# Kernel optimization log

Measured on AMD Instinct MI355X. Metric: run time of the kernel, lower is better.

## Reference

```python
import jax, jax.numpy as jnp
import numpy as np

N = 50000      # nodes
E = 800000     # edges (before self-loops)
H = 4          # heads
C = 64         # hidden_unit per head
IN = 256       # input_dim
OUT = 64       # output_dim
NEG = 0.2      # LeakyReLU slope in GATConv
EPS = 1e-5     # BatchNorm eps


def setup_inputs() -> dict:
    key = jax.random.key(0)
    ks = jax.random.split(key, 12)
    s = 0.05
    HC = H * C
    return {
        'x': jax.random.normal(ks[0], (N, IN), dtype=jnp.float32),
        'edge_index': jax.random.randint(ks[1], (2, E), 0, N, dtype=jnp.int64),
        # GATConv layer 1
        'W1': jax.random.normal(ks[2], (IN, HC), dtype=jnp.float32) * s,
        'att_src1': jax.random.normal(ks[3], (H, C), dtype=jnp.float32) * s,
        'att_dst1': jax.random.normal(ks[4], (H, C), dtype=jnp.float32) * s,
        'b1': jnp.zeros((HC,), jnp.float32),
        # GATConv layer 2
        'W2': jax.random.normal(ks[5], (HC, HC), dtype=jnp.float32) * s,
        'att_src2': jax.random.normal(ks[6], (H, C), dtype=jnp.float32) * s,
        'att_dst2': jax.random.normal(ks[7], (H, C), dtype=jnp.float32) * s,
        'b2': jnp.zeros((HC,), jnp.float32),
        # BatchNorms
        'g1': jnp.ones((HC,), jnp.float32), 'beta1': jnp.zeros((HC,), jnp.float32),
        'g2': jnp.ones((HC,), jnp.float32), 'beta2': jnp.zeros((HC,), jnp.float32),
        # final Linear
        'Wl': jax.random.normal(ks[8], (HC, OUT), dtype=jnp.float32) * s,
        'bl': jnp.zeros((OUT,), jnp.float32),
    }


def gat_layer(x, src, dst, W, a_src, a_dst, b):
    # x: [N, F_in] -> per-head features [N, H, C]
    xh = (x @ W).reshape(-1, H, C)
    alpha_src = jnp.einsum('nhc,hc->nh', xh, a_src)   # [N, H]
    alpha_dst = jnp.einsum('nhc,hc->nh', xh, a_dst)   # [N, H]
    e = jax.nn.leaky_relu(alpha_src[src] + alpha_dst[dst], NEG)  # [Etot, H]
    # segment softmax over edges grouped by destination node
    m = jax.ops.segment_max(e, dst, num_segments=N)              # [N, H]
    ex = jnp.exp(e - m[dst])
    den = jax.ops.segment_sum(ex, dst, num_segments=N)           # [N, H]
    alpha = ex / (den[dst] + 1e-16)                              # [Etot, H]
    # weighted scatter-add aggregation
    out = jax.ops.segment_sum(alpha[:, :, None] * xh[src], dst, num_segments=N)
    return out.reshape(-1, H * C) + b


def batchnorm(x, g, beta):
    mu = x.mean(axis=0)
    var = x.var(axis=0)
    return (x - mu) * jax.lax.rsqrt(var + EPS) * g + beta


def reference(x, edge_index, W1, att_src1, att_dst1, b1,
              W2, att_src2, att_dst2, b2, g1, beta1, g2, beta2, Wl, bl):
    # GATConv adds self-loops by default
    loops = jnp.arange(N, dtype=edge_index.dtype)
    src = jnp.concatenate([edge_index[0], loops])
    dst = jnp.concatenate([edge_index[1], loops])
    h = batchnorm(gat_layer(x, src, dst, W1, att_src1, att_dst1, b1), g1, beta1)
    # dropout is identity in eval mode
    h = batchnorm(gat_layer(h, src, dst, W2, att_src2, att_dst2, b2), g2, beta2)
    emb = h @ Wl + bl
    out = jax.nn.log_softmax(emb, axis=1)
    return (out, emb)
```

## Files before the change

### kernel.cpp

```cpp
#include <hip/hip_runtime.h>
#include <cstdint>

#define NNODES 50000
#define NEDGES 800000
#define ETOT   (NEDGES + NNODES)
#define HEADS 4
#define CH 64
#define HC 256
#define INDIM 256
#define OUTDIM 64
#define NEG_SLOPE 0.2f
#define BN_EPS 1e-5f

typedef unsigned short u16;
typedef __attribute__((ext_vector_type(8))) short short8;
typedef __attribute__((ext_vector_type(4))) float floatx4;

__device__ inline float bf2f(u16 u) {
    union { unsigned int i; float f; } c;
    c.i = ((unsigned int)u) << 16;
    return c.f;
}
__device__ inline u16 f2bf(float f) {
    union { float f; unsigned int i; } c;
    c.f = f;
    unsigned int u = c.i + 0x7fff + ((c.i >> 16) & 1);
    return (u16)(u >> 16);
}
__device__ inline void async16(u16* lds, const u16* g) {
    __builtin_amdgcn_global_load_lds(
        (const __attribute__((address_space(1))) unsigned int*)g,
        (__attribute__((address_space(3))) unsigned int*)lds,
        16, 0, 0);
}


__global__ void hist_kernel(const int* __restrict__ ei, int* __restrict__ cnt) {
    int t = blockIdx.x * blockDim.x + threadIdx.x;
    if (t >= ETOT) return;
    int d = (t < NEDGES) ? ei[NEDGES + t] : (t - NEDGES);
    atomicAdd(&cnt[d], 1);
}

__global__ void scan1_kernel(const int* __restrict__ cnt, int* __restrict__ row_off,
                             int* __restrict__ blockSums) {
    __shared__ int tsum[256];
    const int tid = threadIdx.x;
    const int base = blockIdx.x * 4096 + tid * 16;
    int local[16];
    int run = 0;
#pragma unroll
    for (int i = 0; i < 16; ++i) {
        int idx = base + i;
        int v = (idx < NNODES) ? cnt[idx] : 0;
        local[i] = run;
        run += v;
    }
    tsum[tid] = run;
    __syncthreads();
    for (int d = 1; d < 256; d <<= 1) {
        int v = (tid >= d) ? tsum[tid - d] : 0;
        __syncthreads();
        tsum[tid] += v;
        __syncthreads();
    }
    int excl = (tid == 0) ? 0 : tsum[tid - 1];
#pragma unroll
    for (int i = 0; i < 16; ++i) {
        int idx = base + i;
        if (idx < NNODES) row_off[idx] = excl + local[i];
    }
    if (tid == 0) blockSums[blockIdx.x] = tsum[255];
}

__global__ void scan2_kernel(int* __restrict__ row_off, const int* __restrict__ blockSums,
                             int* __restrict__ nxt) {
    __shared__ int sprefix;
    if (threadIdx.x == 0) {
        int p = 0;
        for (int b = 0; b < (int)blockIdx.x; ++b) p += blockSums[b];
        sprefix = p;
    }
    __syncthreads();
    int prefix = sprefix;
    int base = blockIdx.x * 4096 + threadIdx.x * 16;
#pragma unroll
    for (int i = 0; i < 16; ++i) {
        int idx = base + i;
        if (idx < NNODES) {
            int v = row_off[idx] + prefix;
            row_off[idx] = v;
            nxt[idx] = v;
        }
    }
    if (blockIdx.x == 0 && threadIdx.x == 0) row_off[NNODES] = ETOT;
}

__global__ void fill_csr_kernel(const int* __restrict__ ei, int* __restrict__ nxt,
                                int* __restrict__ csr_src) {
    int t = blockIdx.x * blockDim.x + threadIdx.x;
    if (t >= ETOT) return;
    int s, d;
    if (t < NEDGES) { s = ei[t]; d = ei[NEDGES + t]; }
    else            { s = d = t - NEDGES; }
    int pos = atomicAdd(&nxt[d], 1);
    csr_src[pos] = s;
}


__global__ void castx_kernel(const float* __restrict__ x, u16* __restrict__ xb, int n4) {
    int t = blockIdx.x * blockDim.x + threadIdx.x;
    if (t >= n4) return;
    float4 v = *(const float4*)&x[(size_t)t * 4];
    ushort4 o;
    o.x = f2bf(v.x); o.y = f2bf(v.y); o.z = f2bf(v.z); o.w = f2bf(v.w);
    *(ushort4*)&xb[(size_t)t * 4] = o;
}

__global__ void wcast_kernel(const float* __restrict__ W, u16* __restrict__ Wt,
                             int K, int Ncols) {
    int t = blockIdx.x * blockDim.x + threadIdx.x;
    if (t >= K * Ncols) return;
    int k = t / Ncols, n = t - k * Ncols;
    Wt[n * K + k] = f2bf(W[t]);
}


__global__ __launch_bounds__(256)
void gemm_bf16_kernel(const u16* __restrict__ A, const u16* __restrict__ Bt,
                      u16* __restrict__ Cbf, float* __restrict__ Cf,
                      const float* __restrict__ bias, int M, int Ncols, int K) {
    __shared__ u16 As[128 * 32];
    __shared__ u16 Bs[128 * 32];
    const int tid = threadIdx.x;
    const int wave = tid >> 6, lane = tid & 63;
    const int q15 = lane & 15, quad = lane >> 4;
    const int rowBase = blockIdx.y * 128;
    const int colBase = blockIdx.x * 128;
    const int waveM = (wave >> 1) * 64, waveN = (wave & 1) * 64;

    floatx4 acc[4][4];
    floatx4 zero = {0.f, 0.f, 0.f, 0.f};
#pragma unroll
    for (int i = 0; i < 4; ++i)
#pragma unroll
        for (int j = 0; j < 4; ++j) acc[i][j] = zero;

    for (int kt = 0; kt < K; kt += 32) {
#pragma unroll
        for (int q = 0; q < 2; ++q) {
            int e8 = (wave * 2 + q) * 64 + lane;
            int r = e8 >> 2;
            int c = (e8 & 3) * 8;
            int ar = rowBase + r; if (ar >= M) ar = M - 1;
            async16(&As[(wave * 2 + q) * 512], &A[(size_t)ar * K + kt + c]);
            int br = colBase + r; if (br >= Ncols) br = Ncols - 1;
            async16(&Bs[(wave * 2 + q) * 512], &Bt[(size_t)br * K + kt + c]);
        }
        __syncthreads();

        short8 af[4], bfr[4];
#pragma unroll
        for (int i = 0; i < 4; ++i)
            af[i] = *(const short8*)&As[(waveM + i * 16 + q15) * 32 + quad * 8];
#pragma unroll
        for (int j = 0; j < 4; ++j)
            bfr[j] = *(const short8*)&Bs[(waveN + j * 16 + q15) * 32 + quad * 8];
#pragma unroll
        for (int i = 0; i < 4; ++i)
#pragma unroll
            for (int j = 0; j < 4; ++j)
                acc[i][j] = __builtin_amdgcn_mfma_f32_16x16x32_bf16(af[i], bfr[j], acc[i][j], 0, 0, 0);
        __syncthreads();
    }

#pragma unroll
    for (int i = 0; i < 4; ++i) {
#pragma unroll
        for (int j = 0; j < 4; ++j) {
            int gcol = colBase + waveN + j * 16 + q15;
            if (gcol >= Ncols) continue;
#pragma unroll
            for (int r = 0; r < 4; ++r) {
                int grow = rowBase + waveM + i * 16 + quad * 4 + r;
                if (grow >= M) continue;
                float v = acc[i][j][r];
                if (bias) v += bias[gcol];
                if (Cf)  Cf[(size_t)grow * Ncols + gcol] = v;
                if (Cbf) Cbf[(size_t)grow * Ncols + gcol] = f2bf(v);
            }
        }
    }
}


__global__ void alpha_kernel(const u16* __restrict__ xh,
                             const float* __restrict__ att_src,
                             const float* __restrict__ att_dst,
                             float* __restrict__ as_, float* __restrict__ ad_) {
    int t = blockIdx.x * blockDim.x + threadIdx.x;
    if (t >= NNODES * HEADS) return;
    int n = t >> 2, h = t & 3;
    const u16* xp = xh + (size_t)n * HC + h * CH;
    const float* sp = att_src + h * CH;
    const float* dp = att_dst + h * CH;
    float s = 0.f, d = 0.f;
#pragma unroll
    for (int c = 0; c < CH; c += 4) {
        ushort4 xv = *(const ushort4*)&xp[c];
        float v0 = bf2f(xv.x), v1 = bf2f(xv.y), v2 = bf2f(xv.z), v3 = bf2f(xv.w);
        s += v0 * sp[c] + v1 * sp[c + 1] + v2 * sp[c + 2] + v3 * sp[c + 3];
        d += v0 * dp[c] + v1 * dp[c + 1] + v2 * dp[c + 2] + v3 * dp[c + 3];
    }
    as_[t] = s;
    ad_[t] = d;
}


__global__ __launch_bounds__(256)
void aggregate_kernel(const int* __restrict__ row_off, const int* __restrict__ csr_src,
                      const float* __restrict__ asrc, const float* __restrict__ adst,
                      const u16* __restrict__ xh, const float* __restrict__ bias,
                      u16* __restrict__ out) {
    const int g = threadIdx.x >> 6;
    const int lane = threadIdx.x & 63;
    const int d = blockIdx.x * 4 + g;
    const int h = lane >> 4;
    const int cbase = lane * 4;
    const float adt = adst[d * 4 + h];
    int start = row_off[d], end = row_off[d + 1];
    float a0 = 0.f, a1 = 0.f, a2 = 0.f, a3 = 0.f, den = 0.f;
    int e = start;
    for (; e + 1 < end; e += 2) {
        int s0 = csr_src[e], s1 = csr_src[e + 1];
        float v0 = asrc[s0 * 4 + h] + adt;
        float v1 = asrc[s1 * 4 + h] + adt;
        ushort4 x0 = *(const ushort4*)&xh[(size_t)s0 * HC + cbase];
        ushort4 x1 = *(const ushort4*)&xh[(size_t)s1 * HC + cbase];
        v0 = v0 > 0.f ? v0 : NEG_SLOPE * v0;
        v1 = v1 > 0.f ? v1 : NEG_SLOPE * v1;
        float w0 = __expf(v0), w1 = __expf(v1);
        den += w0 + w1;
        a0 += w0 * bf2f(x0.x) + w1 * bf2f(x1.x);
        a1 += w0 * bf2f(x0.y) + w1 * bf2f(x1.y);
        a2 += w0 * bf2f(x0.z) + w1 * bf2f(x1.z);
        a3 += w0 * bf2f(x0.w) + w1 * bf2f(x1.w);
    }
    if (e < end) {
        int s0 = csr_src[e];
        float v0 = asrc[s0 * 4 + h] + adt;
        ushort4 x0 = *(const ushort4*)&xh[(size_t)s0 * HC + cbase];
        v0 = v0 > 0.f ? v0 : NEG_SLOPE * v0;
        float w0 = __expf(v0);
        den += w0;
        a0 += w0 * bf2f(x0.x);
        a1 += w0 * bf2f(x0.y);
        a2 += w0 * bf2f(x0.z);
        a3 += w0 * bf2f(x0.w);
    }
    float inv = 1.f / (den + 1e-16f);
    ushort4 o;
    o.x = f2bf(a0 * inv + bias[cbase + 0]);
    o.y = f2bf(a1 * inv + bias[cbase + 1]);
    o.z = f2bf(a2 * inv + bias[cbase + 2]);
    o.w = f2bf(a3 * inv + bias[cbase + 3]);
    *(ushort4*)&out[(size_t)d * HC + cbase] = o;
}


__global__ void bn_stats_kernel(const u16* __restrict__ x, float* __restrict__ sums,
                                float* __restrict__ sumsq) {
    int j = threadIdx.x;
    int r0 = blockIdx.x * 128;
    int r1 = min(r0 + 128, NNODES);
    float s = 0.f, s2 = 0.f;
    for (int r = r0; r < r1; ++r) {
        float v = bf2f(x[(size_t)r * HC + j]);
        s += v;
        s2 += v * v;
    }
    atomicAdd(&sums[j], s);
    atomicAdd(&sumsq[j], s2);
}

__global__ void bn_apply_kernel(const u16* __restrict__ x, u16* __restrict__ y,
                                const float* __restrict__ sums, const float* __restrict__ sumsq,
                                const float* __restrict__ g, const float* __restrict__ beta) {
    int t = blockIdx.x * blockDim.x + threadIdx.x;
    if (t >= NNODES * HC / 4) return;
    int j = (t * 4) & (HC - 1);
    ushort4 xv = *(const ushort4*)&x[(size_t)t * 4];
    ushort4 o;
#pragma unroll
    for (int i = 0; i < 4; ++i) {
        float mu = sums[j + i] * (1.f / NNODES);
        float var = sumsq[j + i] * (1.f / NNODES) - mu * mu;
        float v = bf2f(((const u16*)&xv)[i]);
        ((u16*)&o)[i] = f2bf((v - mu) * rsqrtf(var + BN_EPS) * g[j + i] + beta[j + i]);
    }
    *(ushort4*)&y[(size_t)t * 4] = o;
}


__global__ void logsoftmax_kernel(const float* __restrict__ emb, float* __restrict__ out) {
    int row = blockIdx.x * 4 + (threadIdx.x >> 6);
    int lane = threadIdx.x & 63;
    float v = emb[(size_t)row * OUTDIM + lane];
    float m = v;
    for (int off = 32; off > 0; off >>= 1) m = fmaxf(m, __shfl_xor(m, off, 64));
    float e = expf(v - m);
    float s = e;
    for (int off = 32; off > 0; off >>= 1) s += __shfl_xor(s, off, 64);
    out[(size_t)row * OUTDIM + lane] = v - m - logf(s);
}


extern "C" void kernel_launch(void* const* d_in, const int* in_sizes, int n_in,
                              void* d_out, int out_size, void* d_ws, size_t ws_size,
                              hipStream_t stream) {
    const float* x   = (const float*)d_in[0];
    const int*   ei  = (const int*)d_in[1];
    const float* W1  = (const float*)d_in[2];
    const float* at_s1 = (const float*)d_in[3];
    const float* at_d1 = (const float*)d_in[4];
    const float* b1  = (const float*)d_in[5];
    const float* W2  = (const float*)d_in[6];
    const float* at_s2 = (const float*)d_in[7];
    const float* at_d2 = (const float*)d_in[8];
    const float* b2  = (const float*)d_in[9];
    const float* g1  = (const float*)d_in[10];
    const float* be1 = (const float*)d_in[11];
    const float* g2  = (const float*)d_in[12];
    const float* be2 = (const float*)d_in[13];
    const float* Wl  = (const float*)d_in[14];
    const float* bl  = (const float*)d_in[15];

    float* out = (float*)d_out;
    float* emb = out + (size_t)NNODES * OUTDIM;

    char* ws = (char*)d_ws;
    size_t off = 0;
    auto alloc = [&](size_t bytes) {
        void* p = ws + off;
        off += (bytes + 255) & ~(size_t)255;
        return p;
    };
    int*   cnt     = (int*)alloc((size_t)NNODES * 4);
    int*   row_off = (int*)alloc((size_t)(NNODES + 1) * 4);
    int*   nxt     = (int*)alloc((size_t)NNODES * 4);
    int*   bsums   = (int*)alloc(64 * 4);
    int*   csr_src = (int*)alloc((size_t)ETOT * 4);
    float* asrc    = (float*)alloc((size_t)NNODES * 4 * 4);
    float* adst    = (float*)alloc((size_t)NNODES * 4 * 4);
    u16*   x_bf    = (u16*)alloc((size_t)NNODES * HC * 2);
    u16*   xh_bf   = (u16*)alloc((size_t)NNODES * HC * 2);
    u16*   ag_bf   = (u16*)alloc((size_t)NNODES * HC * 2);
    u16*   h_bf    = (u16*)alloc((size_t)NNODES * HC * 2);
    u16*   w1t     = (u16*)alloc((size_t)HC * INDIM * 2);
    u16*   w2t     = (u16*)alloc((size_t)HC * HC * 2);
    u16*   wlt     = (u16*)alloc((size_t)OUTDIM * HC * 2);
    float* bnsum   = (float*)alloc(HC * 4);
    float* bnsq    = (float*)alloc(HC * 4);

    const int scanBlocks = (NNODES + 4095) / 4096;
    const int eBlocks = (ETOT + 255) / 256;

    hipMemsetAsync(cnt, 0, (size_t)NNODES * 4, stream);
    hist_kernel<<<eBlocks, 256, 0, stream>>>(ei, cnt);
    scan1_kernel<<<scanBlocks, 256, 0, stream>>>(cnt, row_off, bsums);
    scan2_kernel<<<scanBlocks, 256, 0, stream>>>(row_off, bsums, nxt);
    fill_csr_kernel<<<eBlocks, 256, 0, stream>>>(ei, nxt, csr_src);

    castx_kernel<<<(NNODES * HC / 4 + 255) / 256, 256, 0, stream>>>(x, x_bf, NNODES * HC / 4);
    wcast_kernel<<<(INDIM * HC + 255) / 256, 256, 0, stream>>>(W1, w1t, INDIM, HC);
    wcast_kernel<<<(HC * HC + 255) / 256, 256, 0, stream>>>(W2, w2t, HC, HC);
    wcast_kernel<<<(HC * OUTDIM + 255) / 256, 256, 0, stream>>>(Wl, wlt, HC, OUTDIM);

    dim3 gemmGrid(2, (NNODES + 127) / 128);
    dim3 gemmGrid3(1, (NNODES + 127) / 128);
    int nhBlocks = (NNODES * HEADS + 255) / 256;
    int vecBlocks = (NNODES * HC / 4 + 255) / 256;
    int statBlocks = (NNODES + 127) / 128;

    gemm_bf16_kernel<<<gemmGrid, 256, 0, stream>>>(x_bf, w1t, xh_bf, nullptr, nullptr,
                                                   NNODES, HC, INDIM);
    alpha_kernel<<<nhBlocks, 256, 0, stream>>>(xh_bf, at_s1, at_d1, asrc, adst);
    aggregate_kernel<<<NNODES / 4, 256, 0, stream>>>(row_off, csr_src, asrc, adst, xh_bf, b1, ag_bf);
    hipMemsetAsync(bnsum, 0, HC * 4, stream);
    hipMemsetAsync(bnsq, 0, HC * 4, stream);
    bn_stats_kernel<<<statBlocks, HC, 0, stream>>>(ag_bf, bnsum, bnsq);
    bn_apply_kernel<<<vecBlocks, 256, 0, stream>>>(ag_bf, h_bf, bnsum, bnsq, g1, be1);

    gemm_bf16_kernel<<<gemmGrid, 256, 0, stream>>>(h_bf, w2t, xh_bf, nullptr, nullptr,
                                                   NNODES, HC, HC);
    alpha_kernel<<<nhBlocks, 256, 0, stream>>>(xh_bf, at_s2, at_d2, asrc, adst);
    aggregate_kernel<<<NNODES / 4, 256, 0, stream>>>(row_off, csr_src, asrc, adst, xh_bf, b2, ag_bf);
    hipMemsetAsync(bnsum, 0, HC * 4, stream);
    hipMemsetAsync(bnsq, 0, HC * 4, stream);
    bn_stats_kernel<<<statBlocks, HC, 0, stream>>>(ag_bf, bnsum, bnsq);
    bn_apply_kernel<<<vecBlocks, 256, 0, stream>>>(ag_bf, h_bf, bnsum, bnsq, g2, be2);

    gemm_bf16_kernel<<<gemmGrid3, 256, 0, stream>>>(h_bf, wlt, nullptr, emb, bl,
                                                    NNODES, OUTDIM, HC);
    logsoftmax_kernel<<<NNODES / 4, 256, 0, stream>>>(emb, out);
}
```

Measured before the change: 599.6 us.

## Fold BatchNorm into next GEMM weights, fuse final linear with log-softmax, reslice aggregation

```diff
diff --git a/kernel.cpp b/kernel.cpp
--- a/kernel.cpp
+++ b/kernel.cpp
@@ -14,6 +14,7 @@
 
 typedef unsigned short u16;
 typedef __attribute__((ext_vector_type(8))) short short8;
+typedef __attribute__((ext_vector_type(8))) unsigned short ushort8v;
 typedef __attribute__((ext_vector_type(4))) float floatx4;
 
 __device__ inline float bf2f(u16 u) {
@@ -128,8 +129,8 @@
 
 __global__ __launch_bounds__(256)
 void gemm_bf16_kernel(const u16* __restrict__ A, const u16* __restrict__ Bt,
-                      u16* __restrict__ Cbf, float* __restrict__ Cf,
-                      const float* __restrict__ bias, int M, int Ncols, int K) {
+                      u16* __restrict__ Cbf, const float* __restrict__ bias,
+                      int M, int Ncols, int K) {
     __shared__ u16 As[128 * 32];
     __shared__ u16 Bs[128 * 32];
     const int tid = threadIdx.x;
@@ -180,14 +181,12 @@
         for (int j = 0; j < 4; ++j) {
             int gcol = colBase + waveN + j * 16 + q15;
             if (gcol >= Ncols) continue;
+            float bv = bias ? bias[gcol] : 0.f;
 #pragma unroll
             for (int r = 0; r < 4; ++r) {
                 int grow = rowBase + waveM + i * 16 + quad * 4 + r;
                 if (grow >= M) continue;
-                float v = acc[i][j][r];
-                if (bias) v += bias[gcol];
-                if (Cf)  Cf[(size_t)grow * Ncols + gcol] = v;
-                if (Cbf) Cbf[(size_t)grow * Ncols + gcol] = f2bf(v);
+                Cbf[(size_t)grow * Ncols + gcol] = f2bf(acc[i][j][r] + bv);
             }
         }
     }
@@ -206,11 +205,14 @@
     const float* dp = att_dst + h * CH;
     float s = 0.f, d = 0.f;
 #pragma unroll
-    for (int c = 0; c < CH; c += 4) {
-        ushort4 xv = *(const ushort4*)&xp[c];
-        float v0 = bf2f(xv.x), v1 = bf2f(xv.y), v2 = bf2f(xv.z), v3 = bf2f(xv.w);
-        s += v0 * sp[c] + v1 * sp[c + 1] + v2 * sp[c + 2] + v3 * sp[c + 3];
-        d += v0 * dp[c] + v1 * dp[c + 1] + v2 * dp[c + 2] + v3 * dp[c + 3];
+    for (int c = 0; c < CH; c += 8) {
+        ushort8v xv = *(const ushort8v*)&xp[c];
+#pragma unroll
+        for (int i = 0; i < 8; ++i) {
+            float v = bf2f(xv[i]);
+            s += v * sp[c + i];
+            d += v * dp[c + i];
+        }
     }
     as_[t] = s;
     ad_[t] = d;
@@ -222,96 +224,170 @@
                       const float* __restrict__ asrc, const float* __restrict__ adst,
                       const u16* __restrict__ xh, const float* __restrict__ bias,
                       u16* __restrict__ out) {
-    const int g = threadIdx.x >> 6;
-    const int lane = threadIdx.x & 63;
-    const int d = blockIdx.x * 4 + g;
-    const int h = lane >> 4;
-    const int cbase = lane * 4;
+    const int slice = blockIdx.x & 7;
+    const int rid = blockIdx.x >> 3;
+    const int slot = threadIdx.x >> 5;
+    const int lane = threadIdx.x & 31;
+    const int d = rid * 8 + slot;
+    const int ch = slice * 32 + lane;
+    const int h = slice >> 1;
     const float adt = adst[d * 4 + h];
-    int start = row_off[d], end = row_off[d + 1];
-    float a0 = 0.f, a1 = 0.f, a2 = 0.f, a3 = 0.f, den = 0.f;
+    const int start = row_off[d], end = row_off[d + 1];
+    const u16* xb = xh + ch;
+    float acc = 0.f, den = 0.f;
     int e = start;
     for (; e + 1 < end; e += 2) {
         int s0 = csr_src[e], s1 = csr_src[e + 1];
         float v0 = asrc[s0 * 4 + h] + adt;
         float v1 = asrc[s1 * 4 + h] + adt;
-        ushort4 x0 = *(const ushort4*)&xh[(size_t)s0 * HC + cbase];
-        ushort4 x1 = *(const ushort4*)&xh[(size_t)s1 * HC + cbase];
+        u16 x0 = xb[(size_t)s0 * HC];
+        u16 x1 = xb[(size_t)s1 * HC];
         v0 = v0 > 0.f ? v0 : NEG_SLOPE * v0;
         v1 = v1 > 0.f ? v1 : NEG_SLOPE * v1;
         float w0 = __expf(v0), w1 = __expf(v1);
         den += w0 + w1;
-        a0 += w0 * bf2f(x0.x) + w1 * bf2f(x1.x);
-        a1 += w0 * bf2f(x0.y) + w1 * bf2f(x1.y);
-        a2 += w0 * bf2f(x0.z) + w1 * bf2f(x1.z);
-        a3 += w0 * bf2f(x0.w) + w1 * bf2f(x1.w);
+        acc += w0 * bf2f(x0) + w1 * bf2f(x1);
     }
     if (e < end) {
         int s0 = csr_src[e];
         float v0 = asrc[s0 * 4 + h] + adt;
-        ushort4 x0 = *(const ushort4*)&xh[(size_t)s0 * HC + cbase];
+        u16 x0 = xb[(size_t)s0 * HC];
         v0 = v0 > 0.f ? v0 : NEG_SLOPE * v0;
         float w0 = __expf(v0);
         den += w0;
-        a0 += w0 * bf2f(x0.x);
-        a1 += w0 * bf2f(x0.y);
-        a2 += w0 * bf2f(x0.z);
-        a3 += w0 * bf2f(x0.w);
-    }
-    float inv = 1.f / (den + 1e-16f);
-    ushort4 o;
-    o.x = f2bf(a0 * inv + bias[cbase + 0]);
-    o.y = f2bf(a1 * inv + bias[cbase + 1]);
-    o.z = f2bf(a2 * inv + bias[cbase + 2]);
-    o.w = f2bf(a3 * inv + bias[cbase + 3]);
-    *(ushort4*)&out[(size_t)d * HC + cbase] = o;
-}
-
-
-__global__ void bn_stats_kernel(const u16* __restrict__ x, float* __restrict__ sums,
-                                float* __restrict__ sumsq) {
-    int j = threadIdx.x;
-    int r0 = blockIdx.x * 128;
-    int r1 = min(r0 + 128, NNODES);
-    float s = 0.f, s2 = 0.f;
-    for (int r = r0; r < r1; ++r) {
-        float v = bf2f(x[(size_t)r * HC + j]);
-        s += v;
-        s2 += v * v;
-    }
-    atomicAdd(&sums[j], s);
-    atomicAdd(&sumsq[j], s2);
-}
-
-__global__ void bn_apply_kernel(const u16* __restrict__ x, u16* __restrict__ y,
-                                const float* __restrict__ sums, const float* __restrict__ sumsq,
-                                const float* __restrict__ g, const float* __restrict__ beta) {
-    int t = blockIdx.x * blockDim.x + threadIdx.x;
-    if (t >= NNODES * HC / 4) return;
-    int j = (t * 4) & (HC - 1);
-    ushort4 xv = *(const ushort4*)&x[(size_t)t * 4];
-    ushort4 o;
+        acc += w0 * bf2f(x0);
+    }
+    out[(size_t)d * HC + ch] = f2bf(acc / (den + 1e-16f) + bias[ch]);
+}
+
+
+__global__ __launch_bounds__(256)
+void bn_stats_kernel(const u16* __restrict__ x, float* __restrict__ stats) {
+    const int tid = threadIdx.x;
+    const int ch = (tid & 31) * 8;
+    float s[8] = {}, s2[8] = {};
+    const size_t total = (size_t)NNODES * HC;
+    const size_t stride = (size_t)256 * 256 * 8;
+    for (size_t f = ((size_t)blockIdx.x * 256 + tid) * 8; f < total; f += stride) {
+        ushort8v v = *(const ushort8v*)&x[f];
+#pragma unroll
+        for (int i = 0; i < 8; ++i) {
+            float t = bf2f(v[i]);
+            s[i] += t;
+            s2[i] += t * t;
+        }
+    }
+#pragma unroll
+    for (int i = 0; i < 8; ++i) {
+        atomicAdd(&stats[ch + i], s[i]);
+        atomicAdd(&stats[256 + ch + i], s2[i]);
+    }
+}
+
+
+__global__ void fold_kernel(const float* __restrict__ W, const float* __restrict__ stats,
+                            const float* __restrict__ g, const float* __restrict__ beta,
+                            const float* __restrict__ baseBias,
+                            u16* __restrict__ Wt, float* __restrict__ biasOut, int Ncols) {
+    __shared__ float sh[256];
+    int b = blockIdx.x;
+    if (b < 256) {
+        float mu = stats[b] * (1.f / NNODES);
+        float var = stats[256 + b] * (1.f / NNODES) - mu * mu;
+        float rg = rsqrtf(var + BN_EPS) * g[b];
+        for (int n = threadIdx.x; n < Ncols; n += 256)
+            Wt[n * 256 + b] = f2bf(W[b * Ncols + n] * rg);
+    } else {
+        int t = threadIdx.x;
+        float mu = stats[t] * (1.f / NNODES);
+        float var = stats[256 + t] * (1.f / NNODES) - mu * mu;
+        float rg = rsqrtf(var + BN_EPS) * g[t];
+        sh[t] = beta[t] - mu * rg;
+        __syncthreads();
+        if (t < Ncols) {
+            float acc = baseBias ? baseBias[t] : 0.f;
+            for (int k = 0; k < 256; ++k) acc += sh[k] * W[k * Ncols + t];
+            biasOut[t] = acc;
+        }
+    }
+}
+
+
+__global__ __launch_bounds__(256)
+void final_ls_kernel(const u16* __restrict__ A, const u16* __restrict__ Bt,
+                     const float* __restrict__ bias,
+                     float* __restrict__ emb, float* __restrict__ out, int M) {
+    __shared__ u16 As[256 * 32];
+    __shared__ u16 Bs[64 * 32];
+    const int tid = threadIdx.x;
+    const int wave = tid >> 6, lane = tid & 63;
+    const int q15 = lane & 15, quad = lane >> 4;
+    const int rowBase = blockIdx.x * 256;
+
+    floatx4 acc[4][4];
+    floatx4 zero = {0.f, 0.f, 0.f, 0.f};
+#pragma unroll
+    for (int i = 0; i < 4; ++i)
+#pragma unroll
+        for (int j = 0; j < 4; ++j) acc[i][j] = zero;
+
+    for (int kt = 0; kt < 256; kt += 32) {
+#pragma unroll
+        for (int rnd = 0; rnd < 4; ++rnd) {
+            int slot = rnd * 256 + wave * 64 + lane;
+            int r = slot >> 2;
+            int c = (slot & 3) * 8;
+            int ar = rowBase + r; if (ar >= M) ar = M - 1;
+            async16(&As[(rnd * 256 + wave * 64) * 8], &A[(size_t)ar * 256 + kt + c]);
+        }
+        {
+            int slot = wave * 64 + lane;
+            int r = slot >> 2;
+            int c = (slot & 3) * 8;
+            async16(&Bs[(wave * 64) * 8], &Bt[(size_t)r * 256 + kt + c]);
+        }
+        __syncthreads();
+
+        short8 af[4], bfr[4];
+#pragma unroll
+        for (int i = 0; i < 4; ++i)
+            af[i] = *(const short8*)&As[(wave * 64 + i * 16 + q15) * 32 + quad * 8];
+#pragma unroll
+        for (int j = 0; j < 4; ++j)
+            bfr[j] = *(const short8*)&Bs[(j * 16 + q15) * 32 + quad * 8];
+#pragma unroll
+        for (int i = 0; i < 4; ++i)
+#pragma unroll
+            for (int j = 0; j < 4; ++j)
+                acc[i][j] = __builtin_amdgcn_mfma_f32_16x16x32_bf16(af[i], bfr[j], acc[i][j], 0, 0, 0);
+        __syncthreads();
+    }
+
 #pragma unroll
     for (int i = 0; i < 4; ++i) {
-        float mu = sums[j + i] * (1.f / NNODES);
-        float var = sumsq[j + i] * (1.f / NNODES) - mu * mu;
-        float v = bf2f(((const u16*)&xv)[i]);
-        ((u16*)&o)[i] = f2bf((v - mu) * rsqrtf(var + BN_EPS) * g[j + i] + beta[j + i]);
-    }
-    *(ushort4*)&y[(size_t)t * 4] = o;
-}
-
-
-__global__ void logsoftmax_kernel(const float* __restrict__ emb, float* __restrict__ out) {
-    int row = blockIdx.x * 4 + (threadIdx.x >> 6);
-    int lane = threadIdx.x & 63;
-    float v = emb[(size_t)row * OUTDIM + lane];
-    float m = v;
-    for (int off = 32; off > 0; off >>= 1) m = fmaxf(m, __shfl_xor(m, off, 64));
-    float e = expf(v - m);
-    float s = e;
-    for (int off = 32; off > 0; off >>= 1) s += __shfl_xor(s, off, 64);
-    out[(size_t)row * OUTDIM + lane] = v - m - logf(s);
+#pragma unroll
+        for (int rr = 0; rr < 4; ++rr) {
+            float v[4];
+#pragma unroll
+            for (int j = 0; j < 4; ++j) v[j] = acc[i][j][rr] + bias[j * 16 + q15];
+            float m = fmaxf(fmaxf(v[0], v[1]), fmaxf(v[2], v[3]));
+#pragma unroll
+            for (int off = 1; off <= 8; off <<= 1) m = fmaxf(m, __shfl_xor(m, off, 64));
+            float s = __expf(v[0] - m) + __expf(v[1] - m) + __expf(v[2] - m) + __expf(v[3] - m);
+#pragma unroll
+            for (int off = 1; off <= 8; off <<= 1) s += __shfl_xor(s, off, 64);
+            float ls = m + logf(s);
+            int grow = rowBase + wave * 64 + i * 16 + quad * 4 + rr;
+            if (grow < M) {
+#pragma unroll
+                for (int j = 0; j < 4; ++j) {
+                    int col = j * 16 + q15;
+                    emb[(size_t)grow * OUTDIM + col] = v[j];
+                    out[(size_t)grow * OUTDIM + col] = v[j] - ls;
+                }
+            }
+        }
+    }
 }
 
 
@@ -355,12 +431,12 @@
     u16*   x_bf    = (u16*)alloc((size_t)NNODES * HC * 2);
     u16*   xh_bf   = (u16*)alloc((size_t)NNODES * HC * 2);
     u16*   ag_bf   = (u16*)alloc((size_t)NNODES * HC * 2);
-    u16*   h_bf    = (u16*)alloc((size_t)NNODES * HC * 2);
     u16*   w1t     = (u16*)alloc((size_t)HC * INDIM * 2);
     u16*   w2t     = (u16*)alloc((size_t)HC * HC * 2);
     u16*   wlt     = (u16*)alloc((size_t)OUTDIM * HC * 2);
-    float* bnsum   = (float*)alloc(HC * 4);
-    float* bnsq    = (float*)alloc(HC * 4);
+    float* stats   = (float*)alloc(512 * 4);
+    float* bias2   = (float*)alloc(HC * 4);
+    float* blp     = (float*)alloc(OUTDIM * 4);
 
     const int scanBlocks = (NNODES + 4095) / 4096;
     const int eBlocks = (ETOT + 255) / 256;
@@ -373,34 +449,23 @@
 
     castx_kernel<<<(NNODES * HC / 4 + 255) / 256, 256, 0, stream>>>(x, x_bf, NNODES * HC / 4);
     wcast_kernel<<<(INDIM * HC + 255) / 256, 256, 0, stream>>>(W1, w1t, INDIM, HC);
-    wcast_kernel<<<(HC * HC + 255) / 256, 256, 0, stream>>>(W2, w2t, HC, HC);
-    wcast_kernel<<<(HC * OUTDIM + 255) / 256, 256, 0, stream>>>(Wl, wlt, HC, OUTDIM);
 
     dim3 gemmGrid(2, (NNODES + 127) / 128);
-    dim3 gemmGrid3(1, (NNODES + 127) / 128);
     int nhBlocks = (NNODES * HEADS + 255) / 256;
-    int vecBlocks = (NNODES * HC / 4 + 255) / 256;
-    int statBlocks = (NNODES + 127) / 128;
-
-    gemm_bf16_kernel<<<gemmGrid, 256, 0, stream>>>(x_bf, w1t, xh_bf, nullptr, nullptr,
-                                                   NNODES, HC, INDIM);
+
+    gemm_bf16_kernel<<<gemmGrid, 256, 0, stream>>>(x_bf, w1t, xh_bf, nullptr, NNODES, HC, INDIM);
     alpha_kernel<<<nhBlocks, 256, 0, stream>>>(xh_bf, at_s1, at_d1, asrc, adst);
-    aggregate_kernel<<<NNODES / 4, 256, 0, stream>>>(row_off, csr_src, asrc, adst, xh_bf, b1, ag_bf);
-    hipMemsetAsync(bnsum, 0, HC * 4, stream);
-    hipMemsetAsync(bnsq, 0, HC * 4, stream);
-    bn_stats_kernel<<<statBlocks, HC, 0, stream>>>(ag_bf, bnsum, bnsq);
-    bn_apply_kernel<<<vecBlocks, 256, 0, stream>>>(ag_bf, h_bf, bnsum, bnsq, g1, be1);
-
-    gemm_bf16_kernel<<<gemmGrid, 256, 0, stream>>>(h_bf, w2t, xh_bf, nullptr, nullptr,
-                                                   NNODES, HC, HC);
+    aggregate_kernel<<<NNODES, 256, 0, stream>>>(row_off, csr_src, asrc, adst, xh_bf, b1, ag_bf);
+    hipMemsetAsync(stats, 0, 512 * 4, stream);
+    bn_stats_kernel<<<256, 256, 0, stream>>>(ag_bf, stats);
+    fold_kernel<<<257, 256, 0, stream>>>(W2, stats, g1, be1, nullptr, w2t, bias2, HC);
+
+    gemm_bf16_kernel<<<gemmGrid, 256, 0, stream>>>(ag_bf, w2t, xh_bf, bias2, NNODES, HC, HC);
     alpha_kernel<<<nhBlocks, 256, 0, stream>>>(xh_bf, at_s2, at_d2, asrc, adst);
-    aggregate_kernel<<<NNODES / 4, 256, 0, stream>>>(row_off, csr_src, asrc, adst, xh_bf, b2, ag_bf);
-    hipMemsetAsync(bnsum, 0, HC * 4, stream);
-    hipMemsetAsync(bnsq, 0, HC * 4, stream);
-    bn_stats_kernel<<<statBlocks, HC, 0, stream>>>(ag_bf, bnsum, bnsq);
-    bn_apply_kernel<<<vecBlocks, 256, 0, stream>>>(ag_bf, h_bf, bnsum, bnsq, g2, be2);
-
-    gemm_bf16_kernel<<<gemmGrid3, 256, 0, stream>>>(h_bf, wlt, nullptr, emb, bl,
-                                                    NNODES, OUTDIM, HC);
-    logsoftmax_kernel<<<NNODES / 4, 256, 0, stream>>>(emb, out);
-}
+    aggregate_kernel<<<NNODES, 256, 0, stream>>>(row_off, csr_src, asrc, adst, xh_bf, b2, ag_bf);
+    hipMemsetAsync(stats, 0, 512 * 4, stream);
+    bn_stats_kernel<<<256, 256, 0, stream>>>(ag_bf, stats);
+    fold_kernel<<<257, 256, 0, stream>>>(Wl, stats, g2, be2, bl, wlt, blp, OUTDIM);
+
+    final_ls_kernel<<<(NNODES + 255) / 256, 256, 0, stream>>>(ag_bf, wlt, blp, emb, out, NNODES);
+}
```

Result: slower. 1.641 ms (+173.8%).
